# Performance work log

Hardware: AMD Instinct MI355X
Metric: run time of the kernel (lower is better)

Reference implementation:

```python
import jax, jax.numpy as jnp
import numpy as np

B, S, D, H = 2, 2048, 1024, 16
HD = D // H  # head_dim = 64
ROPE_BASE = 10000.0
INIT_STD = 0.02


def setup_inputs() -> dict:
    key = jax.random.key(0)
    k1, k2, k3 = jax.random.split(key, 3)
    x = jax.random.normal(k1, (B, S, D), dtype=jnp.float32)
    w_qkv = jax.random.normal(k2, (3 * D, D), dtype=jnp.float32) * INIT_STD
    w_out = jax.random.normal(k3, (D, D), dtype=jnp.float32) * (1.0 / np.sqrt(D))
    b_out = jnp.zeros((D,), dtype=jnp.float32)
    return {"x": x, "w_qkv": w_qkv, "w_out": w_out, "b_out": b_out}


def _rope_cos_sin(s_len, head_dim, dtype):
    theta = 1.0 / ROPE_BASE ** (jnp.arange(0, head_dim, 2, dtype=jnp.float32) / head_dim)
    freqs = jnp.outer(jnp.arange(s_len, dtype=jnp.float32), theta)  # [s, d/2]
    freqs = jnp.concatenate([freqs, freqs], axis=-1)  # [s, d]
    return jnp.cos(freqs).astype(dtype), jnp.sin(freqs).astype(dtype)


def _apply_rope(qk, cos, sin):
    # qk: [b, h, s, d]; rotate-half: (-x2, x1)
    d2 = qk.shape[-1] // 2
    x1, x2 = qk[..., :d2], qk[..., d2:]
    rot = jnp.concatenate([-x2, x1], axis=-1)
    return qk * cos + rot * sin


def reference(x, w_qkv, w_out, b_out):
    b, s, d = x.shape
    qkv = jnp.einsum('bsd,ed->bse', x, w_qkv)  # [b, s, 3D]
    qkv = qkv.reshape(b, s, 3 * H, HD).transpose(0, 2, 1, 3)  # [b, 3h, s, d]
    qk, v = qkv[:, :2 * H], qkv[:, 2 * H:]
    cos, sin = _rope_cos_sin(s, HD, x.dtype)
    qk = _apply_rope(qk, cos, sin)
    q, k = qk[:, :H], qk[:, H:]
    scale = 1.0 / np.sqrt(HD)
    scores = jnp.einsum('bhqd,bhkd->bhqk', q, k) * scale  # [b, h, s, s]
    causal = jnp.tril(jnp.ones((s, s), dtype=bool))
    scores = jnp.where(causal, scores, jnp.finfo(scores.dtype).min)
    attn = jax.nn.softmax(scores, axis=-1)
    o = jnp.einsum('bhqk,bhkd->bhqd', attn, v)  # [b, h, s, d]
    o = o.transpose(0, 2, 1, 3).reshape(b, s, d)
    return jnp.einsum('bsd,ed->bse', o, w_out) + b_out
```

## Files before the change

kernel.cpp:

```cpp
#include <hip/hip_runtime.h>
#include <hip/hip_fp16.h>
#include <math.h>

#define B_  2
#define S_  2048
#define D_  1024
#define H_  16
#define HD_ 64

typedef _Float16  f16;
typedef __attribute__((ext_vector_type(8))) _Float16 f16x8;
typedef __attribute__((ext_vector_type(4))) _Float16 f16x4;
typedef __attribute__((ext_vector_type(4))) float    f32x4;

#define LOG2E 1.4426950408889634f
#define L2_10000_DIV32 0.41524101186092029f

__device__ __forceinline__ float fin(float v) { return (v == v) ? v : 0.0f; }

__device__ __forceinline__ f16x8 cvt8(const float* p) {
  float4 a = *(const float4*)p;
  float4 b = *(const float4*)(p + 4);
  f16x8 h;
  h[0] = (f16)a.x; h[1] = (f16)a.y; h[2] = (f16)a.z; h[3] = (f16)a.w;
  h[4] = (f16)b.x; h[5] = (f16)b.y; h[6] = (f16)b.z; h[7] = (f16)b.w;
  return h;
}

__device__ __forceinline__ int swz64(int r, int c) {
  return r * 64 + ((((c >> 3) ^ (r & 7)) << 3) | (c & 7));
}

#define GLD16(g, l)                                                        \
  __builtin_amdgcn_global_load_lds(                                        \
      (const __attribute__((address_space(1))) void*)(g),                  \
      (__attribute__((address_space(3))) void*)(l), 16, 0, 0)

__global__ void __launch_bounds__(256)
k_cvt3(const float* __restrict__ wq, const float* __restrict__ wo,
       const float* __restrict__ x,
       f16* __restrict__ wqh, f16* __restrict__ woh, f16* __restrict__ xh,
       int doX)
{
  const int NWQ = 3 * D_ * D_ / 4, NWO = D_ * D_ / 4, NX = B_ * S_ * D_ / 4;
  const int n = NWQ + NWO + (doX ? NX : 0);
  for (int i = blockIdx.x * 256 + threadIdx.x; i < n; i += gridDim.x * 256) {
    const float* src; f16* dst; int j;
    if (i < NWQ)            { src = wq; dst = wqh; j = i; }
    else if (i < NWQ + NWO) { src = wo; dst = woh; j = i - NWQ; }
    else                    { src = x;  dst = xh;  j = i - NWQ - NWO; }
    float4 v = ((const float4*)src)[j];
    f16x4 h = {(f16)v.x, (f16)v.y, (f16)v.z, (f16)v.w};
    ((f16x4*)dst)[j] = h;
  }
}

template <bool XF16>
__global__ void __launch_bounds__(256)
k_qkv3(const float* __restrict__ xf, const f16* __restrict__ xh,
       const f16* __restrict__ wqh,
       f16* __restrict__ Qb, f16* __restrict__ Kb, f16* __restrict__ Vt)
{
  __shared__ __align__(16) f16 As[128 * 64];
  __shared__ __align__(16) f16 Bs[128 * 64];
  const int t = threadIdx.x;
  const int w = t >> 6;
  const int lane = t & 63;
  const int ll = lane & 15;
  const int quad = lane >> 4;
  const int wm = w >> 1, wn = w & 1;
  const int row0 = blockIdx.y * 128;
  const int col0 = blockIdx.x * 128;

  const f32x4 fz = {0.f, 0.f, 0.f, 0.f};
  f32x4 acc[4][4];
#pragma unroll
  for (int i = 0; i < 4; ++i)
#pragma unroll
    for (int j = 0; j < 4; ++j) acc[i][j] = fz;

  const int rO = lane >> 3;
  const int gc = (lane & 7) ^ rO;
  const f16* gah2 = xh  + (size_t)(row0 + w * 8 + rO) * D_ + gc * 8;
  const f16* gb2  = wqh + (size_t)(col0 + w * 8 + rO) * D_ + gc * 8;

  const int ldr = t >> 3;
  const int ldk = (t & 7) * 8;
  const float* gaf = xf + (size_t)(row0 + ldr) * D_ + ldk;

  for (int kt = 0; kt < D_; kt += 64) {
    f16x8 ra[4];
    if (!XF16) {
#pragma unroll
      for (int i = 0; i < 4; ++i)
        ra[i] = cvt8(gaf + (size_t)i * 32 * D_ + kt);
    }
    __syncthreads();
    if (XF16) {
#pragma unroll
      for (int i = 0; i < 4; ++i) {
        GLD16(gah2 + (size_t)(i * 32) * D_ + kt, &As[(i * 32 + w * 8) * 64]);
        GLD16(gb2  + (size_t)(i * 32) * D_ + kt, &Bs[(i * 32 + w * 8) * 64]);
      }
    } else {
#pragma unroll
      for (int i = 0; i < 4; ++i) {
        *(f16x8*)&As[swz64(i * 32 + ldr, ldk)] = ra[i];
        GLD16(gb2 + (size_t)(i * 32) * D_ + kt, &Bs[(i * 32 + w * 8) * 64]);
      }
    }
    __syncthreads();
#pragma unroll
    for (int kk = 0; kk < 64; kk += 32) {
      f16x8 a[4], b[4];
#pragma unroll
      for (int mt = 0; mt < 4; ++mt)
        a[mt] = *(const f16x8*)&As[swz64(wm * 64 + mt * 16 + ll, kk + quad * 8)];
#pragma unroll
      for (int nt = 0; nt < 4; ++nt)
        b[nt] = *(const f16x8*)&Bs[swz64(wn * 64 + nt * 16 + ll, kk + quad * 8)];
#pragma unroll
      for (int mt = 0; mt < 4; ++mt)
#pragma unroll
        for (int nt = 0; nt < 4; ++nt)
          acc[mt][nt] = __builtin_amdgcn_mfma_f32_16x16x32_f16(
              a[mt], b[nt], acc[mt][nt], 0, 0, 0);
    }
  }

  const int h3 = (col0 >> 6) + wn;
  if (h3 < 32) {
    f16* dst = (h3 < 16) ? Qb : Kb;
    const int h = (h3 < 16) ? h3 : h3 - 16;
    const float th0 = exp2f(-(float)ll * L2_10000_DIV32);
    const float th1 = exp2f(-(float)(16 + ll) * L2_10000_DIV32);
#pragma unroll
    for (int mt = 0; mt < 4; ++mt) {
#pragma unroll
      for (int r = 0; r < 4; ++r) {
        const int row = row0 + wm * 64 + mt * 16 + quad * 4 + r;
        const int b = row >> 11;
        const int p = row & (S_ - 1);
        f16* base = dst + ((size_t)(b * H_ + h) * S_ + p) * HD_;
        const float fp = (float)p;
        float s0, c0, s1, c1;
        sincosf(fp * th0, &s0, &c0);
        sincosf(fp * th1, &s1, &c1);
        {
          float x1 = acc[mt][0][r], x2 = acc[mt][2][r];
          base[ll]      = (f16)fin(x1 * c0 - x2 * s0);
          base[ll + 32] = (f16)fin(x2 * c0 + x1 * s0);
        }
        {
          float x1 = acc[mt][1][r], x2 = acc[mt][3][r];
          base[16 + ll]      = (f16)fin(x1 * c1 - x2 * s1);
          base[16 + ll + 32] = (f16)fin(x2 * c1 + x1 * s1);
        }
      }
    }
  } else {
    const int hv = h3 - 32;
#pragma unroll
    for (int mt = 0; mt < 4; ++mt)
#pragma unroll
      for (int nt = 0; nt < 4; ++nt)
#pragma unroll
        for (int r = 0; r < 4; ++r) {
          const int row = row0 + wm * 64 + mt * 16 + quad * 4 + r;
          const int b = row >> 11;
          const int p = row & (S_ - 1);
          const int dd = nt * 16 + ll;
          Vt[((size_t)(b * H_ + hv) * HD_ + dd) * S_ + p] = (f16)fin(acc[mt][nt][r]);
        }
  }
}

__device__ __forceinline__ bool softmax_tile4(
    f32x4 sc[4], bool diag, int qloc, int ll, int quad,
    float& mrun, float& lrun, float& alpha, f16* Pt)
{
  if (diag) {
#pragma unroll
    for (int nt = 0; nt < 4; ++nt)
#pragma unroll
      for (int r = 0; r < 4; ++r)
        if ((nt * 16 + quad * 4 + r) > qloc) sc[nt][r] = -3.0e4f;
  }
  float pm = mrun;
#pragma unroll
  for (int nt = 0; nt < 4; ++nt)
#pragma unroll
    for (int r = 0; r < 4; ++r) pm = fmaxf(pm, sc[nt][r]);
  pm = fmaxf(pm, __shfl_xor(pm, 16));
  pm = fmaxf(pm, __shfl_xor(pm, 32));
  const bool resc = !__all(pm <= mrun + 8.0f);
  if (resc) { alpha = exp2f(mrun - pm); mrun = pm; }
  float ps = 0.f;
#pragma unroll
  for (int nt = 0; nt < 4; ++nt) {
    f16x4 pk;
#pragma unroll
    for (int r = 0; r < 4; ++r) {
      float p = exp2f(sc[nt][r] - mrun);
      ps += p;
      pk[r] = (f16)p;
    }
    *(f16x4*)&Pt[swz64(ll, nt * 16 + quad * 4)] = pk;
  }
  ps += __shfl_xor(ps, 16);
  ps += __shfl_xor(ps, 32);
  lrun = (resc ? lrun * alpha : lrun) + ps;
  return resc;
}

__device__ __forceinline__ void write_o4(
    f32x4 acco[4], float lrun, f16* Pt, int ll, int quad, int w,
    int qt, size_t bh, f16* Ob)
{
  const float inv = 1.0f / fmaxf(lrun, 1e-30f);
#pragma unroll
  for (int dg = 0; dg < 4; ++dg) {
    f16x4 ov;
#pragma unroll
    for (int r = 0; r < 4; ++r) ov[r] = (f16)fin(acco[dg][r] * inv);
    *(f16x4*)&Pt[swz64(ll, dg * 16 + quad * 4)] = ov;
  }
#pragma unroll
  for (int s2 = 0; s2 < 2; ++s2) {
    f16x8 o = *(const f16x8*)&Pt[swz64(ll, (quad + 4 * s2) * 8)];
    const size_t row = bh * S_ + qt * 64 + w * 16 + ll;
    *(f16x8*)&Ob[row * HD_ + (quad + 4 * s2) * 8] = o;
  }
}

__global__ void __launch_bounds__(256, 4)
k_attn4(const f16* Qb, const f16* __restrict__ Kb,
        const f16* __restrict__ Vt, f16* Ob)
{
  __shared__ __align__(16) f16 Ks[2][64 * 64];
  __shared__ __align__(16) f16 Vs[2][64 * 64];
  __shared__ __align__(16) f16 Ps[4][16 * 64];

  const int t = threadIdx.x;
  const int w = t >> 6;
  const int lane = t & 63;
  const int ll = lane & 15;
  const int quad = lane >> 4;
  const int bx = blockIdx.x;
  const int base = (bx & 1) ? 31 - (bx >> 1) : (bx >> 1);
  const int qt = ((int)blockIdx.y < 8) ? base : 31 - base;
  const int h = blockIdx.y;
  const int b = blockIdx.z;
  const size_t bh = (size_t)b * H_ + h;
  const f16* Qg = Qb + bh * S_ * HD_;
  const f16* Kg = Kb + bh * S_ * HD_;
  const f16* Vg = Vt + bh * HD_ * S_;

  f16x8 bq[2];
  {
    const f16 hsc = (f16)(0.125f * LOG2E);
#pragma unroll
    for (int k2 = 0; k2 < 2; ++k2) {
      bq[k2] = *(const f16x8*)(Qg + (size_t)(qt * 64 + w * 16 + ll) * HD_ + k2 * 32 + quad * 8);
#pragma unroll
      for (int e = 0; e < 8; ++e) bq[k2][e] *= hsc;
    }
  }
  const int sr = t >> 2;
  const int scc = (t & 3) * 16;
  {
    f16x8 a0 = *(const f16x8*)(Kg + (size_t)sr * HD_ + scc);
    f16x8 a1 = *(const f16x8*)(Kg + (size_t)sr * HD_ + scc + 8);
    f16x8 b0 = *(const f16x8*)(Vg + (size_t)sr * S_ + scc);
    f16x8 b1 = *(const f16x8*)(Vg + (size_t)sr * S_ + scc + 8);
    *(f16x8*)&Ks[0][swz64(sr, scc)]     = a0;
    *(f16x8*)&Ks[0][swz64(sr, scc + 8)] = a1;
    *(f16x8*)&Vs[0][swz64(sr, scc)]     = b0;
    *(f16x8*)&Vs[0][swz64(sr, scc + 8)] = b1;
  }
  __syncthreads();

  const f32x4 fz = {0.f, 0.f, 0.f, 0.f};
  f32x4 acco[4] = {fz, fz, fz, fz};
  float m = -3.0e4f, l = 0.f;
  const int qloc = w * 16 + ll;
  f16* Pt = &Ps[w][0];

  for (int kt = 0; kt <= qt; ++kt) {
    const int cur = kt & 1;
    const bool pre = (kt < qt);
    f16x8 nk0, nk1, nv0, nv1;
    if (pre) {
      const int kn = (kt + 1) * 64;
      nk0 = *(const f16x8*)(Kg + (size_t)(kn + sr) * HD_ + scc);
      nk1 = *(const f16x8*)(Kg + (size_t)(kn + sr) * HD_ + scc + 8);
      nv0 = *(const f16x8*)(Vg + (size_t)sr * S_ + kn + scc);
      nv1 = *(const f16x8*)(Vg + (size_t)sr * S_ + kn + scc + 8);
    }
    const f16* Kc = Ks[cur];
    const f16* Vc = Vs[cur];

    f16x8 ak[2][4];
#pragma unroll
    for (int k2 = 0; k2 < 2; ++k2)
#pragma unroll
      for (int nt = 0; nt < 4; ++nt)
        ak[k2][nt] = *(const f16x8*)&Kc[swz64(nt * 16 + ll, k2 * 32 + quad * 8)];

    f32x4 s[4] = {fz, fz, fz, fz};
#pragma unroll
    for (int k2 = 0; k2 < 2; ++k2)
#pragma unroll
      for (int nt = 0; nt < 4; ++nt)
        s[nt] = __builtin_amdgcn_mfma_f32_16x16x32_f16(ak[k2][nt], bq[k2], s[nt], 0, 0, 0);

    f16x8 av[2][4];
#pragma unroll
    for (int k2 = 0; k2 < 2; ++k2)
#pragma unroll
      for (int dg = 0; dg < 4; ++dg)
        av[k2][dg] = *(const f16x8*)&Vc[swz64(dg * 16 + ll, k2 * 32 + quad * 8)];

    float alpha;
    const bool resc = softmax_tile4(s, kt == qt, qloc, ll, quad, m, l, alpha, Pt);
    if (resc) {
#pragma unroll
      for (int dg = 0; dg < 4; ++dg)
#pragma unroll
        for (int r = 0; r < 4; ++r) acco[dg][r] *= alpha;
    }
#pragma unroll
    for (int k2 = 0; k2 < 2; ++k2) {
      f16x8 bp = *(const f16x8*)&Pt[swz64(ll, k2 * 32 + quad * 8)];
#pragma unroll
      for (int dg = 0; dg < 4; ++dg)
        acco[dg] = __builtin_amdgcn_mfma_f32_16x16x32_f16(av[k2][dg], bp, acco[dg], 0, 0, 0);
    }

    if (pre) {
      *(f16x8*)&Ks[1 - cur][swz64(sr, scc)]     = nk0;
      *(f16x8*)&Ks[1 - cur][swz64(sr, scc + 8)] = nk1;
      *(f16x8*)&Vs[1 - cur][swz64(sr, scc)]     = nv0;
      *(f16x8*)&Vs[1 - cur][swz64(sr, scc + 8)] = nv1;
    }
    __syncthreads();
  }

  write_o4(acco, l, Pt, ll, quad, w, qt, bh, Ob);
}

__global__ void __launch_bounds__(256)
k_out3(const f16* __restrict__ Ob, const f16* __restrict__ Wh,
       const float* __restrict__ bias, float* __restrict__ out)
{
  __shared__ __align__(16) f16 As[64 * 64];
  __shared__ __align__(16) f16 Bs[128 * 64];
  const int t = threadIdx.x;
  const int w = t >> 6;
  const int lane = t & 63;
  const int ll = lane & 15;
  const int quad = lane >> 4;
  const int wm = w >> 1, wn = w & 1;
  const int row0 = blockIdx.y * 64;
  const int col0 = blockIdx.x * 128;
  const int bb = row0 >> 11;
  const int s0 = row0 & (S_ - 1);

  const f32x4 fz = {0.f, 0.f, 0.f, 0.f};
  f32x4 acc[2][4];
#pragma unroll
  for (int i = 0; i < 2; ++i)
#pragma unroll
    for (int j = 0; j < 4; ++j) acc[i][j] = fz;

  const int rO = lane >> 3;
  const int gc = (lane & 7) ^ rO;
  const f16* gb2 = Wh + (size_t)(col0 + w * 8 + rO) * D_ + gc * 8;

  for (int kt = 0; kt < 16; ++kt) {
    const f16* ga2 = Ob + (((size_t)(bb * H_ + kt)) * S_ + s0 + w * 8 + rO) * HD_ + gc * 8;
    __syncthreads();
#pragma unroll
    for (int i = 0; i < 2; ++i)
      GLD16(ga2 + (size_t)(i * 32) * HD_, &As[(i * 32 + w * 8) * 64]);
#pragma unroll
    for (int i = 0; i < 4; ++i)
      GLD16(gb2 + (size_t)(i * 32) * D_ + kt * 64, &Bs[(i * 32 + w * 8) * 64]);
    __syncthreads();
#pragma unroll
    for (int kk = 0; kk < 64; kk += 32) {
      f16x8 a[2], b[4];
#pragma unroll
      for (int mt = 0; mt < 2; ++mt)
        a[mt] = *(const f16x8*)&As[swz64(wm * 32 + mt * 16 + ll, kk + quad * 8)];
#pragma unroll
      for (int nt = 0; nt < 4; ++nt)
        b[nt] = *(const f16x8*)&Bs[swz64(wn * 64 + nt * 16 + ll, kk + quad * 8)];
#pragma unroll
      for (int mt = 0; mt < 2; ++mt)
#pragma unroll
        for (int nt = 0; nt < 4; ++nt)
          acc[mt][nt] = __builtin_amdgcn_mfma_f32_16x16x32_f16(
              a[mt], b[nt], acc[mt][nt], 0, 0, 0);
    }
  }

#pragma unroll
  for (int mt = 0; mt < 2; ++mt)
#pragma unroll
    for (int r = 0; r < 4; ++r) {
      const int row = row0 + wm * 32 + mt * 16 + quad * 4 + r;
#pragma unroll
      for (int nt = 0; nt < 4; ++nt) {
        const int col = col0 + wn * 64 + nt * 16 + ll;
        out[(size_t)row * D_ + col] = fin(acc[mt][nt][r] + bias[col]);
      }
    }
}

extern "C" void kernel_launch(void* const* d_in, const int* in_sizes, int n_in,
                              void* d_out, int out_size, void* d_ws, size_t ws_size,
                              hipStream_t stream) {
  const float* x    = (const float*)d_in[0];
  const float* wqkv = (const float*)d_in[1];
  const float* wout = (const float*)d_in[2];
  const float* bout = (const float*)d_in[3];
  float* out = (float*)d_out;

  char* ws = (char*)d_ws;
  f16* wqh = (f16*)(ws);
  f16* Qb  = (f16*)(ws + 6291456);
  f16* Kb  = (f16*)(ws + 14680064);
  f16* Vt  = (f16*)(ws + 23068672);
  f16* woh = (f16*)(ws + 31457280);
  const bool bigws = ws_size >= (size_t)41943040;
  f16* xh  = (f16*)(ws + 33554432);

  k_cvt3<<<2048, 256, 0, stream>>>(wqkv, wout, x, wqh, woh, xh, bigws ? 1 : 0);
  if (bigws)
    k_qkv3<true><<<dim3(3 * D_ / 128, (B_ * S_) / 128), 256, 0, stream>>>(
        x, xh, wqh, Qb, Kb, Vt);
  else
    k_qkv3<false><<<dim3(3 * D_ / 128, (B_ * S_) / 128), 256, 0, stream>>>(
        x, xh, wqh, Qb, Kb, Vt);
  k_attn4<<<dim3(32, H_, B_), 256, 0, stream>>>(Qb, Kb, Vt, Qb );
  k_out3<<<dim3(D_ / 128, (B_ * S_) / 64), 256, 0, stream>>>(
      Qb, woh, bout, out);
}
```

Before: 184.5 us.

## Precompute RoPE table and load V fragments directly from global in attention

The conversion kernel now also builds a cos/sin table (stored temporarily in the output buffer), and the QKV epilogue reads it instead of calling sincosf for every row. The attention kernel stops staging V through double-buffered LDS and loads the V fragments straight from global memory each iteration. This frees LDS, which may improve occupancy, and removes the LDS stores and reads for V. The cost is uncoalesced-ish global latency on V that is no longer prefetched a tile ahead, plus table loads in the QKV epilogue.

```diff
diff --git a/kernel.cpp b/kernel.cpp
--- a/kernel.cpp
+++ b/kernel.cpp
@@ -40,7 +40,7 @@
 k_cvt3(const float* __restrict__ wq, const float* __restrict__ wo,
        const float* __restrict__ x,
        f16* __restrict__ wqh, f16* __restrict__ woh, f16* __restrict__ xh,
-       int doX)
+       float2* __restrict__ tab, int doX)
 {
   const int NWQ = 3 * D_ * D_ / 4, NWO = D_ * D_ / 4, NX = B_ * S_ * D_ / 4;
   const int n = NWQ + NWO + (doX ? NX : 0);
@@ -53,12 +53,19 @@
     f16x4 h = {(f16)v.x, (f16)v.y, (f16)v.z, (f16)v.w};
     ((f16x4*)dst)[j] = h;
   }
+  for (int i = blockIdx.x * 256 + threadIdx.x; i < S_ * 32; i += gridDim.x * 256) {
+    const int p = i >> 5, j = i & 31;
+    const float th = exp2f(-(float)j * L2_10000_DIV32);
+    float s, c;
+    sincosf((float)p * th, &s, &c);
+    tab[i] = make_float2(c, s);
+  }
 }
 
 template <bool XF16>
 __global__ void __launch_bounds__(256)
 k_qkv3(const float* __restrict__ xf, const f16* __restrict__ xh,
-       const f16* __restrict__ wqh,
+       const f16* __restrict__ wqh, const float2* __restrict__ tab,
        f16* __restrict__ Qb, f16* __restrict__ Kb, f16* __restrict__ Vt)
 {
   __shared__ __align__(16) f16 As[128 * 64];
@@ -132,8 +139,6 @@
   if (h3 < 32) {
     f16* dst = (h3 < 16) ? Qb : Kb;
     const int h = (h3 < 16) ? h3 : h3 - 16;
-    const float th0 = exp2f(-(float)ll * L2_10000_DIV32);
-    const float th1 = exp2f(-(float)(16 + ll) * L2_10000_DIV32);
 #pragma unroll
     for (int mt = 0; mt < 4; ++mt) {
 #pragma unroll
@@ -142,19 +147,17 @@
         const int b = row >> 11;
         const int p = row & (S_ - 1);
         f16* base = dst + ((size_t)(b * H_ + h) * S_ + p) * HD_;
-        const float fp = (float)p;
-        float s0, c0, s1, c1;
-        sincosf(fp * th0, &s0, &c0);
-        sincosf(fp * th1, &s1, &c1);
+        const float2 cs0 = tab[p * 32 + ll];
+        const float2 cs1 = tab[p * 32 + 16 + ll];
         {
           float x1 = acc[mt][0][r], x2 = acc[mt][2][r];
-          base[ll]      = (f16)fin(x1 * c0 - x2 * s0);
-          base[ll + 32] = (f16)fin(x2 * c0 + x1 * s0);
+          base[ll]      = (f16)fin(x1 * cs0.x - x2 * cs0.y);
+          base[ll + 32] = (f16)fin(x2 * cs0.x + x1 * cs0.y);
         }
         {
           float x1 = acc[mt][1][r], x2 = acc[mt][3][r];
-          base[16 + ll]      = (f16)fin(x1 * c1 - x2 * s1);
-          base[16 + ll + 32] = (f16)fin(x2 * c1 + x1 * s1);
+          base[16 + ll]      = (f16)fin(x1 * cs1.x - x2 * cs1.y);
+          base[16 + ll + 32] = (f16)fin(x2 * cs1.x + x1 * cs1.y);
         }
       }
     }
@@ -234,11 +237,10 @@
 }
 
 __global__ void __launch_bounds__(256, 4)
-k_attn4(const f16* Qb, const f16* __restrict__ Kb,
+k_attn5(const f16* Qb, const f16* __restrict__ Kb,
         const f16* __restrict__ Vt, f16* Ob)
 {
   __shared__ __align__(16) f16 Ks[2][64 * 64];
-  __shared__ __align__(16) f16 Vs[2][64 * 64];
   __shared__ __align__(16) f16 Ps[4][16 * 64];
 
   const int t = threadIdx.x;
@@ -271,12 +273,8 @@
   {
     f16x8 a0 = *(const f16x8*)(Kg + (size_t)sr * HD_ + scc);
     f16x8 a1 = *(const f16x8*)(Kg + (size_t)sr * HD_ + scc + 8);
-    f16x8 b0 = *(const f16x8*)(Vg + (size_t)sr * S_ + scc);
-    f16x8 b1 = *(const f16x8*)(Vg + (size_t)sr * S_ + scc + 8);
     *(f16x8*)&Ks[0][swz64(sr, scc)]     = a0;
     *(f16x8*)&Ks[0][swz64(sr, scc + 8)] = a1;
-    *(f16x8*)&Vs[0][swz64(sr, scc)]     = b0;
-    *(f16x8*)&Vs[0][swz64(sr, scc + 8)] = b1;
   }
   __syncthreads();
 
@@ -289,16 +287,20 @@
   for (int kt = 0; kt <= qt; ++kt) {
     const int cur = kt & 1;
     const bool pre = (kt < qt);
-    f16x8 nk0, nk1, nv0, nv1;
+    f16x8 nk0, nk1;
     if (pre) {
       const int kn = (kt + 1) * 64;
       nk0 = *(const f16x8*)(Kg + (size_t)(kn + sr) * HD_ + scc);
       nk1 = *(const f16x8*)(Kg + (size_t)(kn + sr) * HD_ + scc + 8);
-      nv0 = *(const f16x8*)(Vg + (size_t)sr * S_ + kn + scc);
-      nv1 = *(const f16x8*)(Vg + (size_t)sr * S_ + kn + scc + 8);
     }
     const f16* Kc = Ks[cur];
-    const f16* Vc = Vs[cur];
+
+    f16x8 av[2][4];
+#pragma unroll
+    for (int k2 = 0; k2 < 2; ++k2)
+#pragma unroll
+      for (int dg = 0; dg < 4; ++dg)
+        av[k2][dg] = *(const f16x8*)(Vg + (size_t)(dg * 16 + ll) * S_ + kt * 64 + k2 * 32 + quad * 8);
 
     f16x8 ak[2][4];
 #pragma unroll
@@ -313,13 +315,6 @@
 #pragma unroll
       for (int nt = 0; nt < 4; ++nt)
         s[nt] = __builtin_amdgcn_mfma_f32_16x16x32_f16(ak[k2][nt], bq[k2], s[nt], 0, 0, 0);
-
-    f16x8 av[2][4];
-#pragma unroll
-    for (int k2 = 0; k2 < 2; ++k2)
-#pragma unroll
-      for (int dg = 0; dg < 4; ++dg)
-        av[k2][dg] = *(const f16x8*)&Vc[swz64(dg * 16 + ll, k2 * 32 + quad * 8)];
 
     float alpha;
     const bool resc = softmax_tile4(s, kt == qt, qloc, ll, quad, m, l, alpha, Pt);
@@ -340,8 +335,6 @@
     if (pre) {
       *(f16x8*)&Ks[1 - cur][swz64(sr, scc)]     = nk0;
       *(f16x8*)&Ks[1 - cur][swz64(sr, scc + 8)] = nk1;
-      *(f16x8*)&Vs[1 - cur][swz64(sr, scc)]     = nv0;
-      *(f16x8*)&Vs[1 - cur][swz64(sr, scc + 8)] = nv1;
     }
     __syncthreads();
   }
@@ -435,15 +428,16 @@
   f16* woh = (f16*)(ws + 31457280);
   const bool bigws = ws_size >= (size_t)41943040;
   f16* xh  = (f16*)(ws + 33554432);
-
-  k_cvt3<<<2048, 256, 0, stream>>>(wqkv, wout, x, wqh, woh, xh, bigws ? 1 : 0);
+  float2* tab = (float2*)d_out;
+
+  k_cvt3<<<2048, 256, 0, stream>>>(wqkv, wout, x, wqh, woh, xh, tab, bigws ? 1 : 0);
   if (bigws)
     k_qkv3<true><<<dim3(3 * D_ / 128, (B_ * S_) / 128), 256, 0, stream>>>(
-        x, xh, wqh, Qb, Kb, Vt);
+        x, xh, wqh, tab, Qb, Kb, Vt);
   else
     k_qkv3<false><<<dim3(3 * D_ / 128, (B_ * S_) / 128), 256, 0, stream>>>(
-        x, xh, wqh, Qb, Kb, Vt);
-  k_attn4<<<dim3(32, H_, B_), 256, 0, stream>>>(Qb, Kb, Vt, Qb );
+        x, xh, wqh, tab, Qb, Kb, Vt);
+  k_attn5<<<dim3(32, H_, B_), 256, 0, stream>>>(Qb, Kb, Vt, Qb );
   k_out3<<<dim3(D_ / 128, (B_ * S_) / 64), 256, 0, stream>>>(
       Qb, woh, bout, out);
 }
```

Measured after the change: 210.0 us. +13.8%, slower.
